# Optimization experiments

Measured on AMD Instinct MI355X. Metric: run time of the kernel, lower is better.

The kernel has to match this reference:

```python
import jax, jax.numpy as jnp
import numpy as np

EMBED_DIM = 1024
NUM_HEADS = 16
HEAD_DIM = EMBED_DIM // NUM_HEADS  # 64
BATCH = 2
SEQ = 2048
BASE = 10000.0
EPS = 1e-5


def setup_inputs() -> dict:
    key = jax.random.key(0)
    ks = jax.random.split(key, 8)
    d, h, hd = EMBED_DIM, NUM_HEADS, HEAD_DIM
    s = d ** -0.5
    x = jax.random.normal(ks[0], (BATCH, SEQ, d), dtype=jnp.float32)
    Wq = jax.random.normal(ks[1], (d, d), dtype=jnp.float32) * s
    Wk = jax.random.normal(ks[2], (d, d), dtype=jnp.float32) * s
    Wv = jax.random.normal(ks[3], (d, d), dtype=jnp.float32) * s
    Wo = jax.random.normal(ks[4], (d, d), dtype=jnp.float32) * s
    G1 = jax.random.normal(ks[5], (d, hd), dtype=jnp.float32) * s
    G2 = jax.random.normal(ks[6], (hd, d), dtype=jnp.float32) * (hd ** -0.5)
    gamma = jnp.ones((d,), jnp.float32)
    beta = jnp.zeros((d,), jnp.float32)
    # TransNormer-style cosine LRPE angles: theta[h, 1, hd]
    theta = jnp.asarray(
        (BASE ** (-2.0 / (h * hd) * np.arange(h * hd))).reshape(h, 1, hd),
        dtype=jnp.float32,
    )
    return {"x": x, "Wq": Wq, "Wk": Wk, "Wv": Wv, "Wo": Wo,
            "G1": G1, "G2": G2, "gamma": gamma, "beta": beta, "theta": theta}


def _lrpe(t, theta, offset=0):
    # t: [b, h, n, hd]; theta: [h, 1, hd] -> [b, h, n, 2*hd]
    n = t.shape[-2]
    idx = (jnp.arange(n) + offset).reshape(1, -1, 1).astype(theta.dtype)
    ang = theta * idx  # [h, n, hd], broadcasts over batch
    return jnp.concatenate([t * jnp.cos(ang), t * jnp.sin(ang)], axis=-1)


def reference(x, Wq, Wk, Wv, Wo, G1, G2, gamma, beta, theta):
    b, n, d = x.shape
    h, hd = NUM_HEADS, HEAD_DIM
    q = jax.nn.silu(x @ Wq)
    k = jax.nn.silu(x @ Wk)
    v = x @ Wv
    split = lambda t: t.reshape(b, n, h, hd).transpose(0, 2, 1, 3)  # b h n hd
    q, k, v = split(q), split(k), split(v)
    q = _lrpe(q, theta)  # b h n 2*hd
    k = _lrpe(k, theta)
    mask = jnp.tril(jnp.ones((n, n), dtype=x.dtype))
    energy = jnp.einsum('bhnd,bhmd->bhnm', q, k) * mask  # causal masked QK^T
    out = jnp.einsum('bhnm,bhmd->bhnd', energy, v)
    out = out.transpose(0, 2, 1, 3).reshape(b, n, d)
    out = out @ Wo
    gate = jax.nn.sigmoid((x @ G1) @ G2)
    out = out * gate
    mu = jnp.mean(out, axis=-1, keepdims=True)
    var = jnp.var(out, axis=-1, keepdims=True)
    out = (out - mu) / jnp.sqrt(var + EPS) * gamma + beta
    return out
```

## Files before the change

### kernel.cpp

```cpp
#include <hip/hip_runtime.h>
#include <hip/hip_bf16.h>
#include <cstdint>
#include <cstddef>

typedef __bf16 bf16_t;
typedef __bf16 bf16x4 __attribute__((ext_vector_type(4)));
typedef __bf16 bf16x8 __attribute__((ext_vector_type(8)));
typedef float  f32x4  __attribute__((ext_vector_type(4)));

__device__ __forceinline__ void async_copy16(const void* g, void* l) {
  __builtin_amdgcn_global_load_lds(
      (const __attribute__((address_space(1))) void*)g,
      (__attribute__((address_space(3))) void*)l, 16, 0, 0);
}


__global__ void f32_to_bf16_kernel(const float* __restrict__ in, bf16_t* __restrict__ out) {
  size_t i = ((size_t)blockIdx.x * blockDim.x + threadIdx.x) * 8;
  float4 a = *(const float4*)(in + i);
  float4 b = *(const float4*)(in + i + 4);
  bf16x8 o;
  o[0] = (__bf16)a.x; o[1] = (__bf16)a.y; o[2] = (__bf16)a.z; o[3] = (__bf16)a.w;
  o[4] = (__bf16)b.x; o[5] = (__bf16)b.y; o[6] = (__bf16)b.z; o[7] = (__bf16)b.w;
  *(bf16x8*)(out + i) = o;
}

__global__ void transpose4_kernel(const float* __restrict__ w0, const float* __restrict__ w1,
                                  const float* __restrict__ w2, const float* __restrict__ w3,
                                  bf16_t* __restrict__ o0, bf16_t* __restrict__ o1,
                                  bf16_t* __restrict__ o2, bf16_t* __restrict__ o3) {
  int z = blockIdx.z;
  const float* in = (z == 0) ? w0 : (z == 1) ? w1 : (z == 2) ? w2 : w3;
  bf16_t* out = (z == 0) ? o0 : (z == 1) ? o1 : (z == 2) ? o2 : o3;
  __shared__ float tile[32][33];
  int x = threadIdx.x, y = threadIdx.y;
  int c0 = blockIdx.x * 32, r0 = blockIdx.y * 32;
  #pragma unroll
  for (int i = 0; i < 32; i += 8) tile[y + i][x] = in[(size_t)(r0 + y + i) * 1024 + c0 + x];
  __syncthreads();
  #pragma unroll
  for (int i = 0; i < 32; i += 8)
    out[(size_t)(c0 + y + i) * 1024 + r0 + x] = (__bf16)tile[x][y + i];
}

__global__ void transpose_f32_bf16_kernel(const float* __restrict__ in, bf16_t* __restrict__ out,
                                          int rows, int cols) {
  __shared__ float tile[32][33];
  int x = threadIdx.x, y = threadIdx.y;
  int c0 = blockIdx.x * 32, r0 = blockIdx.y * 32;
  #pragma unroll
  for (int i = 0; i < 32; i += 8) tile[y + i][x] = in[(size_t)(r0 + y + i) * cols + c0 + x];
  __syncthreads();
  #pragma unroll
  for (int i = 0; i < 32; i += 8)
    out[(size_t)(c0 + y + i) * rows + r0 + x] = (__bf16)tile[x][y + i];
}


__global__ __launch_bounds__(256) void lrpe_table2_kernel(const float* __restrict__ theta,
                                                          float2* __restrict__ tab) {
  int col = blockIdx.x * 256 + threadIdx.x;
  int n0 = blockIdx.y * 32;
  float th = theta[col];
  float c0, s0, dc, ds;
  sincosf(th * (float)n0, &s0, &c0);
  sincosf(th, &ds, &dc);
  float2* p = tab + (size_t)n0 * 1024 + col;
  #pragma unroll
  for (int i = 0; i < 32; ++i) {
    *p = make_float2(c0, s0);
    float c1 = c0 * dc - s0 * ds;
    float s1 = s0 * dc + c0 * ds;
    c0 = c1; s0 = s1;
    p += 1024;
  }
}


__global__ __launch_bounds__(256) void gemm_qkv(
    const bf16_t* __restrict__ A, const bf16_t* __restrict__ Bt,
    const float2* __restrict__ lrpe,
    bf16_t* __restrict__ qrb, bf16_t* __restrict__ krb, bf16_t* __restrict__ vbb) {
  constexpr int K = 1024, BK = 64, GX = 24;
  __shared__ alignas(16) bf16_t lA[128 * BK];
  __shared__ alignas(16) bf16_t lB[128 * BK];
  const int tid = threadIdx.x, w = tid >> 6, l = tid & 63;
  const int wm = w >> 1, wn = w & 1;
  const int l15 = l & 15, lg = l >> 4;
  const int cpx = gridDim.x >> 3;
  const int id = blockIdx.x;
  const int sw = (id & 7) * cpx + (id >> 3);
  const int by = sw / GX, bx = sw % GX;
  const int r0 = by * 128, c0 = bx * 128;
  const int srow_l = l >> 3, sslot = l & 7;
  f32x4 acc[4][4] = {};
  for (int k0 = 0; k0 < K; k0 += BK) {
    #pragma unroll
    for (int i = 0; i < 4; ++i) {
      int seg = i * 4 + w, row = seg * 8 + srow_l, xs = sslot ^ (row & 7);
      async_copy16(A + (size_t)(r0 + row) * K + k0 + xs * 8, lA + seg * 512);
    }
    #pragma unroll
    for (int i = 0; i < 4; ++i) {
      int seg = i * 4 + w, row = seg * 8 + srow_l, xs = sslot ^ (row & 7);
      async_copy16(Bt + (size_t)(c0 + row) * K + k0 + xs * 8, lB + seg * 512);
    }
    __syncthreads();
    #pragma unroll
    for (int ks = 0; ks < 2; ++ks) {
      bf16x8 af[4], bfr[4];
      #pragma unroll
      for (int mt = 0; mt < 4; ++mt) {
        int row = wm * 64 + mt * 16 + l15;
        int s = (ks * 4 + lg) ^ (row & 7);
        af[mt] = *(const bf16x8*)(lA + row * BK + s * 8);
      }
      #pragma unroll
      for (int nt = 0; nt < 4; ++nt) {
        int row = wn * 64 + nt * 16 + l15;
        int s = (ks * 4 + lg) ^ (row & 7);
        bfr[nt] = *(const bf16x8*)(lB + row * BK + s * 8);
      }
      #pragma unroll
      for (int mt = 0; mt < 4; ++mt)
        #pragma unroll
        for (int nt = 0; nt < 4; ++nt)
          acc[mt][nt] = __builtin_amdgcn_mfma_f32_16x16x32_bf16(af[mt], bfr[nt], acc[mt][nt], 0, 0, 0);
    }
    __syncthreads();
  }
  #pragma unroll
  for (int mt = 0; mt < 4; ++mt)
  #pragma unroll
  for (int nt = 0; nt < 4; ++nt)
  #pragma unroll
  for (int r = 0; r < 4; ++r) {
    int grow = r0 + wm * 64 + mt * 16 + lg * 4 + r;
    int gcol = c0 + wn * 64 + nt * 16 + l15;
    float v = acc[mt][nt][r];
    int sect = gcol >> 10, col = gcol & 1023;
    int b = grow >> 11, n = grow & 2047;
    int h = col >> 6, d = col & 63;
    if (sect == 2) {
      vbb[((size_t)(b * 16 + h) * 2048 + n) * 64 + d] = (__bf16)v;
    } else {
      float sv = v / (1.f + expf(-v));
      float2 cs = lrpe[(size_t)n * 1024 + col];
      bf16_t* dst = sect ? krb : qrb;
      size_t base = ((size_t)(b * 16 + h) * 2048 + n) * 128 + d;
      dst[base] = (__bf16)(sv * cs.x);
      dst[base + 64] = (__bf16)(sv * cs.y);
    }
  }
}


__global__ __launch_bounds__(256) void gemm_wo(
    const bf16_t* __restrict__ A, const bf16_t* __restrict__ Bt,
    const bf16_t* __restrict__ xg1b, const bf16_t* __restrict__ G2T,
    float* __restrict__ fout) {
  constexpr int K = 1024, BK = 64, GX = 8;
  __shared__ alignas(16) bf16_t lA[64 * BK];
  __shared__ alignas(16) bf16_t lB[128 * BK];
  const int tid = threadIdx.x, w = tid >> 6, l = tid & 63;
  const int wm = w >> 1, wn = w & 1;
  const int l15 = l & 15, lg = l >> 4;
  const int cpx = gridDim.x >> 3;
  const int id = blockIdx.x;
  const int sw = (id & 7) * cpx + (id >> 3);
  const int by = sw / GX, bx = sw % GX;
  const int r0 = by * 64, c0 = bx * 128;
  const int srow_l = l >> 3, sslot = l & 7;
  f32x4 acc[2][4] = {};
  for (int k0 = 0; k0 < K; k0 += BK) {
    #pragma unroll
    for (int i = 0; i < 2; ++i) {
      int seg = i * 4 + w, row = seg * 8 + srow_l, xs = sslot ^ (row & 7);
      async_copy16(A + (size_t)(r0 + row) * K + k0 + xs * 8, lA + seg * 512);
    }
    #pragma unroll
    for (int i = 0; i < 4; ++i) {
      int seg = i * 4 + w, row = seg * 8 + srow_l, xs = sslot ^ (row & 7);
      async_copy16(Bt + (size_t)(c0 + row) * K + k0 + xs * 8, lB + seg * 512);
    }
    __syncthreads();
    #pragma unroll
    for (int ks = 0; ks < 2; ++ks) {
      bf16x8 af[2], bfr[4];
      #pragma unroll
      for (int mt = 0; mt < 2; ++mt) {
        int row = wm * 32 + mt * 16 + l15;
        int s = (ks * 4 + lg) ^ (row & 7);
        af[mt] = *(const bf16x8*)(lA + row * BK + s * 8);
      }
      #pragma unroll
      for (int nt = 0; nt < 4; ++nt) {
        int row = wn * 64 + nt * 16 + l15;
        int s = (ks * 4 + lg) ^ (row & 7);
        bfr[nt] = *(const bf16x8*)(lB + row * BK + s * 8);
      }
      #pragma unroll
      for (int mt = 0; mt < 2; ++mt)
        #pragma unroll
        for (int nt = 0; nt < 4; ++nt)
          acc[mt][nt] = __builtin_amdgcn_mfma_f32_16x16x32_bf16(af[mt], bfr[nt], acc[mt][nt], 0, 0, 0);
    }
    __syncthreads();
  }
  #pragma unroll
  for (int i = 0; i < 2; ++i) {
    int seg = i * 4 + w, row = seg * 8 + srow_l, xs = sslot ^ (row & 7);
    async_copy16(xg1b + (size_t)(r0 + row) * 64 + xs * 8, lA + seg * 512);
  }
  #pragma unroll
  for (int i = 0; i < 4; ++i) {
    int seg = i * 4 + w, row = seg * 8 + srow_l, xs = sslot ^ (row & 7);
    async_copy16(G2T + (size_t)(c0 + row) * 64 + xs * 8, lB + seg * 512);
  }
  __syncthreads();
  f32x4 acc2[2][4] = {};
  #pragma unroll
  for (int ks = 0; ks < 2; ++ks) {
    bf16x8 af[2], bfr[4];
    #pragma unroll
    for (int mt = 0; mt < 2; ++mt) {
      int row = wm * 32 + mt * 16 + l15;
      int s = (ks * 4 + lg) ^ (row & 7);
      af[mt] = *(const bf16x8*)(lA + row * BK + s * 8);
    }
    #pragma unroll
    for (int nt = 0; nt < 4; ++nt) {
      int row = wn * 64 + nt * 16 + l15;
      int s = (ks * 4 + lg) ^ (row & 7);
      bfr[nt] = *(const bf16x8*)(lB + row * BK + s * 8);
    }
    #pragma unroll
    for (int mt = 0; mt < 2; ++mt)
      #pragma unroll
      for (int nt = 0; nt < 4; ++nt)
        acc2[mt][nt] = __builtin_amdgcn_mfma_f32_16x16x32_bf16(af[mt], bfr[nt], acc2[mt][nt], 0, 0, 0);
  }
  #pragma unroll
  for (int mt = 0; mt < 2; ++mt)
  #pragma unroll
  for (int nt = 0; nt < 4; ++nt)
  #pragma unroll
  for (int r = 0; r < 4; ++r) {
    int grow = r0 + wm * 32 + mt * 16 + lg * 4 + r;
    int gcol = c0 + wn * 64 + nt * 16 + l15;
    float g = 1.f / (1.f + expf(-acc2[mt][nt][r]));
    fout[(size_t)grow * 1024 + gcol] = acc[mt][nt][r] * g;
  }
}


__global__ __launch_bounds__(512) void xg1_kernel(const float* __restrict__ x,
                                                  const float* __restrict__ G1,
                                                  bf16_t* __restrict__ xg1b) {
  int r0 = blockIdx.x * 8, t = threadIdx.x;
  __shared__ float xs[8][1024];
  __shared__ float part[8][8][64];
  const float* xr = x + (size_t)r0 * 1024;
  #pragma unroll
  for (int i = 0; i < 4; ++i)
    ((float4*)&xs[0][0])[t + i * 512] = ((const float4*)xr)[t + i * 512];
  __syncthreads();
  int cc = t & 63, kh = t >> 6;
  float acc[8] = {0, 0, 0, 0, 0, 0, 0, 0};
  for (int k = kh * 128; k < kh * 128 + 128; ++k) {
    float g = G1[(size_t)k * 64 + cc];
    #pragma unroll
    for (int rr = 0; rr < 8; ++rr) acc[rr] += xs[rr][k] * g;
  }
  #pragma unroll
  for (int rr = 0; rr < 8; ++rr) part[kh][rr][cc] = acc[rr];
  __syncthreads();
  int r2 = t >> 6, c2 = t & 63;
  float s2 = 0.f;
  #pragma unroll
  for (int j = 0; j < 8; ++j) s2 += part[j][r2][c2];
  xg1b[(size_t)(r0 + r2) * 64 + c2] = (__bf16)s2;
}


__global__ __launch_bounds__(256) void chunk_state_kernel(const bf16_t* __restrict__ kr,
                                                          const bf16_t* __restrict__ vb,
                                                          float* __restrict__ cstate) {
  const int c = blockIdx.x, bh = blockIdx.y;
  const int tid = threadIdx.x, w = tid >> 6, l = tid & 63;
  const int l15 = l & 15, lg = l >> 4;
  __shared__ alignas(16) bf16_t kT[128][144];
  __shared__ alignas(16) bf16_t vT[64][144];
  const bf16_t* kb = kr + ((size_t)bh * 2048 + c * 128) * 128;
  const bf16_t* vsrc = vb + ((size_t)bh * 2048 + c * 128) * 64;
  {
    int m = tid >> 1, half = tid & 1;
    #pragma unroll
    for (int i = 0; i < 8; ++i) {
      bf16x8 kv = *(const bf16x8*)(kb + (size_t)m * 128 + half * 64 + i * 8);
      #pragma unroll
      for (int j = 0; j < 8; ++j) kT[half * 64 + i * 8 + j][m] = kv[j];
    }
    int dv0 = half * 32;
    #pragma unroll
    for (int i = 0; i < 4; ++i) {
      bf16x8 vv = *(const bf16x8*)(vsrc + (size_t)m * 64 + dv0 + i * 8);
      #pragma unroll
      for (int j = 0; j < 8; ++j) vT[dv0 + i * 8 + j][m] = vv[j];
    }
  }
  __syncthreads();
  f32x4 acc[4][2] = {};
  #pragma unroll
  for (int km = 0; km < 4; ++km) {
    bf16x8 a[4], b2[2];
    #pragma unroll
    for (int mt = 0; mt < 4; ++mt) a[mt] = *(const bf16x8*)&vT[mt * 16 + l15][km * 32 + lg * 8];
    #pragma unroll
    for (int nt = 0; nt < 2; ++nt) b2[nt] = *(const bf16x8*)&kT[w * 32 + nt * 16 + l15][km * 32 + lg * 8];
    #pragma unroll
    for (int mt = 0; mt < 4; ++mt)
      #pragma unroll
      for (int nt = 0; nt < 2; ++nt)
        acc[mt][nt] = __builtin_amdgcn_mfma_f32_16x16x32_bf16(a[mt], b2[nt], acc[mt][nt], 0, 0, 0);
  }
  float* out = cstate + ((size_t)bh * 16 + c) * 8192;
  #pragma unroll
  for (int mt = 0; mt < 4; ++mt)
  #pragma unroll
  for (int nt = 0; nt < 2; ++nt)
  #pragma unroll
  for (int r = 0; r < 4; ++r) {
    int dv = mt * 16 + lg * 4 + r;
    int dk = w * 32 + nt * 16 + l15;
    out[dv * 128 + dk] = acc[mt][nt][r];
  }
}


__global__ __launch_bounds__(256) void prefix_state_kernel(const float* __restrict__ cstate,
                                                           bf16_t* __restrict__ pstate) {
  int bh = blockIdx.y;
  int e0 = blockIdx.x * 1024 + threadIdx.x * 4;
  const float* cs = cstate + (size_t)bh * 16 * 8192 + e0;
  bf16_t* ps = pstate + (size_t)bh * 16 * 8192 + e0;
  float ax = 0.f, ay = 0.f, az = 0.f, aw = 0.f;
  #pragma unroll
  for (int c = 0; c < 16; ++c) {
    bf16x4 o;
    o[0] = (__bf16)ax; o[1] = (__bf16)ay; o[2] = (__bf16)az; o[3] = (__bf16)aw;
    *(bf16x4*)(ps + (size_t)c * 8192) = o;
    float4 v = *(const float4*)(cs + (size_t)c * 8192);
    ax += v.x; ay += v.y; az += v.z; aw += v.w;
  }
}


__global__ __launch_bounds__(256) void attn_kernel(const bf16_t* __restrict__ qr,
                                                   const bf16_t* __restrict__ kr,
                                                   const bf16_t* __restrict__ vb,
                                                   const bf16_t* __restrict__ pstate,
                                                   bf16_t* __restrict__ attno) {
  const int c = blockIdx.x, bh = blockIdx.y;
  const int b = bh >> 4, h = bh & 15;
  const int tid = threadIdx.x, w = tid >> 6, l = tid & 63;
  const int wr = w >> 1, wc = w & 1, l15 = l & 15, lg = l >> 4;
  __shared__ alignas(16) bf16_t e_lds[128][144];
  __shared__ alignas(16) bf16_t vT[64][144];
  const int n0 = c * 128;
  const bf16_t* qb = qr + (size_t)bh * 2048 * 128;
  const bf16_t* kb = kr + (size_t)bh * 2048 * 128;
  const bf16_t* vsrc = vb + ((size_t)bh * 2048 + n0) * 64;
  const bf16_t* sb = pstate + ((size_t)bh * 16 + c) * 8192;
  {
    int m = tid >> 1, dv0 = (tid & 1) * 32;
    #pragma unroll
    for (int i = 0; i < 4; ++i) {
      bf16x8 vv = *(const bf16x8*)(vsrc + (size_t)m * 64 + dv0 + i * 8);
      #pragma unroll
      for (int j = 0; j < 8; ++j) vT[dv0 + i * 8 + j][m] = vv[j];
    }
  }
  f32x4 acc_e[4][4] = {};
  f32x4 acc[4][2] = {};
  #pragma unroll
  for (int kk = 0; kk < 4; ++kk) {
    bf16x8 af[4], bk[4], bs[2];
    #pragma unroll
    for (int mt = 0; mt < 4; ++mt)
      af[mt] = *(const bf16x8*)(qb + (size_t)(n0 + wr * 64 + mt * 16 + l15) * 128 + kk * 32 + lg * 8);
    #pragma unroll
    for (int nt = 0; nt < 4; ++nt)
      bk[nt] = *(const bf16x8*)(kb + (size_t)(n0 + wc * 64 + nt * 16 + l15) * 128 + kk * 32 + lg * 8);
    #pragma unroll
    for (int nt = 0; nt < 2; ++nt)
      bs[nt] = *(const bf16x8*)(sb + (size_t)(wc * 32 + nt * 16 + l15) * 128 + kk * 32 + lg * 8);
    #pragma unroll
    for (int mt = 0; mt < 4; ++mt) {
      #pragma unroll
      for (int nt = 0; nt < 4; ++nt)
        acc_e[mt][nt] = __builtin_amdgcn_mfma_f32_16x16x32_bf16(af[mt], bk[nt], acc_e[mt][nt], 0, 0, 0);
      #pragma unroll
      for (int nt = 0; nt < 2; ++nt)
        acc[mt][nt] = __builtin_amdgcn_mfma_f32_16x16x32_bf16(af[mt], bs[nt], acc[mt][nt], 0, 0, 0);
    }
  }
  #pragma unroll
  for (int mt = 0; mt < 4; ++mt)
  #pragma unroll
  for (int nt = 0; nt < 4; ++nt)
  #pragma unroll
  for (int r = 0; r < 4; ++r) {
    int row = wr * 64 + mt * 16 + lg * 4 + r;
    int col = wc * 64 + nt * 16 + l15;
    float v = (col <= row) ? acc_e[mt][nt][r] : 0.f;
    e_lds[row][col] = (__bf16)v;
  }
  __syncthreads();
  #pragma unroll
  for (int km = 0; km < 4; ++km) {
    bf16x8 af[4], bv[2];
    #pragma unroll
    for (int mt = 0; mt < 4; ++mt)
      af[mt] = *(const bf16x8*)&e_lds[wr * 64 + mt * 16 + l15][km * 32 + lg * 8];
    #pragma unroll
    for (int nt = 0; nt < 2; ++nt)
      bv[nt] = *(const bf16x8*)&vT[wc * 32 + nt * 16 + l15][km * 32 + lg * 8];
    #pragma unroll
    for (int mt = 0; mt < 4; ++mt)
      #pragma unroll
      for (int nt = 0; nt < 2; ++nt)
        acc[mt][nt] = __builtin_amdgcn_mfma_f32_16x16x32_bf16(af[mt], bv[nt], acc[mt][nt], 0, 0, 0);
  }
  #pragma unroll
  for (int mt = 0; mt < 4; ++mt)
  #pragma unroll
  for (int nt = 0; nt < 2; ++nt)
  #pragma unroll
  for (int r = 0; r < 4; ++r) {
    int row = n0 + wr * 64 + mt * 16 + lg * 4 + r;
    int dv = wc * 32 + nt * 16 + l15;
    attno[((size_t)b * 2048 + row) * 1024 + h * 64 + dv] = (__bf16)acc[mt][nt][r];
  }
}


__global__ __launch_bounds__(256) void ln_kernel(const float* __restrict__ owo,
                                                 const float* __restrict__ gamma,
                                                 const float* __restrict__ beta,
                                                 float* __restrict__ out) {
  int r = blockIdx.x, t = threadIdx.x;
  const float4 o = ((const float4*)(owo + (size_t)r * 1024))[t];
  float sum = o.x + o.y + o.z + o.w;
  float ss = o.x * o.x + o.y * o.y + o.z * o.z + o.w * o.w;
  #pragma unroll
  for (int off = 32; off > 0; off >>= 1) {
    sum += __shfl_down(sum, off);
    ss += __shfl_down(ss, off);
  }
  __shared__ float rs[4], rq[4];
  if ((t & 63) == 0) { rs[t >> 6] = sum; rq[t >> 6] = ss; }
  __syncthreads();
  sum = rs[0] + rs[1] + rs[2] + rs[3];
  ss = rq[0] + rq[1] + rq[2] + rq[3];
  float mean = sum * (1.f / 1024.f);
  float var = ss * (1.f / 1024.f) - mean * mean;
  float inv = rsqrtf(var + 1e-5f);
  const float4 g = ((const float4*)gamma)[t];
  const float4 be = ((const float4*)beta)[t];
  float4 res;
  res.x = (o.x - mean) * inv * g.x + be.x;
  res.y = (o.y - mean) * inv * g.y + be.y;
  res.z = (o.z - mean) * inv * g.z + be.z;
  res.w = (o.w - mean) * inv * g.w + be.w;
  ((float4*)(out + (size_t)r * 1024))[t] = res;
}


extern "C" void kernel_launch(void* const* d_in, const int* in_sizes, int n_in,
                              void* d_out, int out_size, void* d_ws, size_t ws_size,
                              hipStream_t stream) {
  const float* x = (const float*)d_in[0];
  const float* Wq = (const float*)d_in[1];
  const float* Wk = (const float*)d_in[2];
  const float* Wv = (const float*)d_in[3];
  const float* Wo = (const float*)d_in[4];
  const float* G1 = (const float*)d_in[5];
  const float* G2 = (const float*)d_in[6];
  const float* gamma = (const float*)d_in[7];
  const float* beta = (const float*)d_in[8];
  const float* theta = (const float*)d_in[9];

  char* w8 = (char*)d_ws;
  size_t off = 0;
  auto take = [&](size_t n) { char* p = w8 + off; off += (n + 255) & ~(size_t)255; return (void*)p; };

  bf16_t* xb    = (bf16_t*)take((size_t)4096 * 1024 * 2);
  bf16_t* qkvT  = (bf16_t*)take((size_t)3072 * 1024 * 2);
  bf16_t* WoT   = (bf16_t*)take((size_t)1024 * 1024 * 2);
  bf16_t* G2T   = (bf16_t*)take((size_t)1024 * 64 * 2);
  bf16_t* xg1b  = (bf16_t*)take((size_t)4096 * 64 * 2);
  bf16_t* qrb   = (bf16_t*)take((size_t)32 * 2048 * 128 * 2);
  bf16_t* krb   = (bf16_t*)take((size_t)32 * 2048 * 128 * 2);
  bf16_t* vbb   = (bf16_t*)take((size_t)32 * 2048 * 64 * 2);
  float*  cst   = (float*)take((size_t)32 * 16 * 8192 * 4);
  bf16_t* pst   = (bf16_t*)take((size_t)32 * 16 * 8192 * 2);
  float*  owo   = (float*)take((size_t)4096 * 1024 * 4);
  bf16_t* attno = xb;
  float2* lrpe  = (float2*)owo;

  dim3 tb(32, 8);
  f32_to_bf16_kernel<<<2048, 256, 0, stream>>>(x, xb);
  transpose4_kernel<<<dim3(32, 32, 4), tb, 0, stream>>>(
      Wq, Wk, Wv, Wo, qkvT, qkvT + (size_t)1024 * 1024, qkvT + (size_t)2048 * 1024, WoT);
  transpose_f32_bf16_kernel<<<dim3(32, 2), tb, 0, stream>>>(G2, G2T, 64, 1024);
  xg1_kernel<<<512, 512, 0, stream>>>(x, G1, xg1b);
  lrpe_table2_kernel<<<dim3(4, 64), 256, 0, stream>>>(theta, lrpe);

  gemm_qkv<<<768, 256, 0, stream>>>(xb, qkvT, lrpe, qrb, krb, vbb);

  chunk_state_kernel<<<dim3(16, 32), 256, 0, stream>>>(krb, vbb, cst);
  prefix_state_kernel<<<dim3(8, 32), 256, 0, stream>>>(cst, pst);

  attn_kernel<<<dim3(16, 32), 256, 0, stream>>>(qrb, krb, vbb, pst, attno);

  gemm_wo<<<512, 256, 0, stream>>>(attno, WoT, xg1b, G2T, owo);

  ln_kernel<<<4096, 256, 0, stream>>>(owo, gamma, beta, (float*)d_out);
}
```

Baseline: 163.5 us.

## Enlarge QKV GEMM tile to 256x256 with double-buffered async LDS pipeline

The QKV projection GEMM moves from 128x128 tiles with 4 waves to 256x256 tiles with 8 waves. It double-buffers the shared-memory staging so the next K-slice loads while the current one computes, using explicit vmcnt waits and barriers. It also raises wave priority around the MFMA block. Larger tiles increase data reuse and cut global traffic, but the grid drops to 192 blocks on a 256-CU device, and register pressure rises with 128 accumulator registers per thread.

```diff
diff --git a/kernel.cpp b/kernel.cpp
--- a/kernel.cpp
+++ b/kernel.cpp
@@ -77,65 +77,91 @@
 }
 
 
-__global__ __launch_bounds__(256) void gemm_qkv(
+__global__ __launch_bounds__(512, 2) void gemm_qkv8(
     const bf16_t* __restrict__ A, const bf16_t* __restrict__ Bt,
     const float2* __restrict__ lrpe,
     bf16_t* __restrict__ qrb, bf16_t* __restrict__ krb, bf16_t* __restrict__ vbb) {
-  constexpr int K = 1024, BK = 64, GX = 24;
-  __shared__ alignas(16) bf16_t lA[128 * BK];
-  __shared__ alignas(16) bf16_t lB[128 * BK];
+  constexpr int K = 1024, BK = 64, T = K / BK;
+  constexpr int BM = 256, BN = 256, GX = 12;
+  __shared__ alignas(16) bf16_t lA[2][BM * BK];
+  __shared__ alignas(16) bf16_t lB[2][BN * BK];
   const int tid = threadIdx.x, w = tid >> 6, l = tid & 63;
-  const int wm = w >> 1, wn = w & 1;
+  const int wm = w >> 2, wn = w & 3;
   const int l15 = l & 15, lg = l >> 4;
   const int cpx = gridDim.x >> 3;
   const int id = blockIdx.x;
   const int sw = (id & 7) * cpx + (id >> 3);
   const int by = sw / GX, bx = sw % GX;
-  const int r0 = by * 128, c0 = bx * 128;
+  const int r0 = by * BM, c0 = bx * BN;
   const int srow_l = l >> 3, sslot = l & 7;
-  f32x4 acc[4][4] = {};
-  for (int k0 = 0; k0 < K; k0 += BK) {
+
+  f32x4 acc[8][4] = {};
+
+  auto stage = [&](int d, int t) {
+    int k0 = t * BK;
     #pragma unroll
     for (int i = 0; i < 4; ++i) {
-      int seg = i * 4 + w, row = seg * 8 + srow_l, xs = sslot ^ (row & 7);
-      async_copy16(A + (size_t)(r0 + row) * K + k0 + xs * 8, lA + seg * 512);
+      int seg = i * 8 + w, row = seg * 8 + srow_l, xs = sslot ^ (row & 7);
+      async_copy16(A + (size_t)(r0 + row) * K + k0 + xs * 8, &lA[d][seg * 512]);
     }
     #pragma unroll
     for (int i = 0; i < 4; ++i) {
-      int seg = i * 4 + w, row = seg * 8 + srow_l, xs = sslot ^ (row & 7);
-      async_copy16(Bt + (size_t)(c0 + row) * K + k0 + xs * 8, lB + seg * 512);
-    }
-    __syncthreads();
+      int seg = i * 8 + w, row = seg * 8 + srow_l, xs = sslot ^ (row & 7);
+      async_copy16(Bt + (size_t)(c0 + row) * K + k0 + xs * 8, &lB[d][seg * 512]);
+    }
+  };
+  auto compute = [&](int d) {
     #pragma unroll
     for (int ks = 0; ks < 2; ++ks) {
-      bf16x8 af[4], bfr[4];
-      #pragma unroll
-      for (int mt = 0; mt < 4; ++mt) {
-        int row = wm * 64 + mt * 16 + l15;
+      bf16x8 af[8], bfr[4];
+      #pragma unroll
+      for (int mt = 0; mt < 8; ++mt) {
+        int row = wm * 128 + mt * 16 + l15;
         int s = (ks * 4 + lg) ^ (row & 7);
-        af[mt] = *(const bf16x8*)(lA + row * BK + s * 8);
+        af[mt] = *(const bf16x8*)(&lA[d][row * BK + s * 8]);
       }
       #pragma unroll
       for (int nt = 0; nt < 4; ++nt) {
         int row = wn * 64 + nt * 16 + l15;
         int s = (ks * 4 + lg) ^ (row & 7);
-        bfr[nt] = *(const bf16x8*)(lB + row * BK + s * 8);
+        bfr[nt] = *(const bf16x8*)(&lB[d][row * BK + s * 8]);
       }
-      #pragma unroll
-      for (int mt = 0; mt < 4; ++mt)
+      __builtin_amdgcn_s_setprio(1);
+      #pragma unroll
+      for (int mt = 0; mt < 8; ++mt)
         #pragma unroll
         for (int nt = 0; nt < 4; ++nt)
           acc[mt][nt] = __builtin_amdgcn_mfma_f32_16x16x32_bf16(af[mt], bfr[nt], acc[mt][nt], 0, 0, 0);
-    }
-    __syncthreads();
-  }
-  #pragma unroll
-  for (int mt = 0; mt < 4; ++mt)
+      __builtin_amdgcn_s_setprio(0);
+    }
+  };
+
+  stage(0, 0);
+  stage(1, 1);
+  for (int t = 0; t < T - 1; ++t) {
+    int d = t & 1;
+    asm volatile("s_waitcnt vmcnt(8)" ::: "memory");
+    __builtin_amdgcn_s_barrier();
+    __builtin_amdgcn_sched_barrier(0);
+    compute(d);
+    asm volatile("s_waitcnt lgkmcnt(0)" ::: "memory");
+    __builtin_amdgcn_sched_barrier(0);
+    __builtin_amdgcn_s_barrier();
+    __builtin_amdgcn_sched_barrier(0);
+    if (t + 2 < T) stage(d, t + 2);
+  }
+  asm volatile("s_waitcnt vmcnt(0)" ::: "memory");
+  __builtin_amdgcn_s_barrier();
+  __builtin_amdgcn_sched_barrier(0);
+  compute((T - 1) & 1);
+
+  #pragma unroll
+  for (int mt = 0; mt < 8; ++mt)
   #pragma unroll
   for (int nt = 0; nt < 4; ++nt)
   #pragma unroll
   for (int r = 0; r < 4; ++r) {
-    int grow = r0 + wm * 64 + mt * 16 + lg * 4 + r;
+    int grow = r0 + wm * 128 + mt * 16 + lg * 4 + r;
     int gcol = c0 + wn * 64 + nt * 16 + l15;
     float v = acc[mt][nt][r];
     int sect = gcol >> 10, col = gcol & 1023;
@@ -517,7 +543,7 @@
   xg1_kernel<<<512, 512, 0, stream>>>(x, G1, xg1b);
   lrpe_table2_kernel<<<dim3(4, 64), 256, 0, stream>>>(theta, lrpe);
 
-  gemm_qkv<<<768, 256, 0, stream>>>(xb, qkvT, lrpe, qrb, krb, vbb);
+  gemm_qkv8<<<192, 512, 0, stream>>>(xb, qkvT, lrpe, qrb, krb, vbb);
 
   chunk_state_kernel<<<dim3(16, 32), 256, 0, stream>>>(krb, vbb, cst);
   prefix_state_kernel<<<dim3(8, 32), 256, 0, stream>>>(cst, pst);
```

Measured after the change: 168.6 us. +3.1%, slower.
